# Performance work log

Measured on AMD Instinct MI355X. Metric: run time of the kernel, lower is better.

The kernel has to match this reference:

```python
import jax, jax.numpy as jnp
import numpy as np
from jax import lax

N, IN_DIM, OUT_DIM, E, K = 100000, 128, 128, 600000, 3

def _xavier(key, shape):
    fan_out, fan_in = shape[0], shape[1]
    limit = float(np.sqrt(6.0 / (fan_in + fan_out)))
    return jax.random.uniform(key, shape, jnp.float32, -limit, limit)

def setup_inputs() -> dict:
    key = jax.random.key(0)
    ks = jax.random.split(key, 8)
    x = jax.random.normal(ks[0], (N, IN_DIM), jnp.float32)
    edge_index0 = jax.random.randint(ks[1], (2, E), 0, N, jnp.int64)
    edge_index1 = jax.random.randint(ks[2], (2, E), 0, N, jnp.int64)
    # relation Linear weights, torch layout [out_dim, in_dim]
    W_rel = jnp.stack([_xavier(ks[3], (OUT_DIM, IN_DIM)), _xavier(ks[4], (OUT_DIM, IN_DIM))])
    W_self = _xavier(ks[5], (OUT_DIM, IN_DIM))
    # Conv1d weight [out_ch, in_ch, k], bias [out_ch]
    fan = OUT_DIM * K
    conv_w = jax.random.uniform(ks[6], (OUT_DIM, OUT_DIM, K), jnp.float32, -1.0/np.sqrt(fan), 1.0/np.sqrt(fan))
    conv_b = jax.random.uniform(ks[7], (OUT_DIM,), jnp.float32, -1.0/np.sqrt(fan), 1.0/np.sqrt(fan))
    return {"x": x, "edge_index0": edge_index0, "edge_index1": edge_index1,
            "W_rel": W_rel, "W_self": W_self, "conv_w": conv_w, "conv_b": conv_b}

def reference(x, edge_index0, edge_index1, W_rel, W_self, conv_w, conv_b):
    num_nodes = x.shape[0]
    agg = jnp.zeros((num_nodes, W_rel.shape[1]), x.dtype)
    # per-relation: gather source feats -> linear -> scatter_add into target rows
    for ei, W in ((edge_index0, W_rel[0]), (edge_index1, W_rel[1])):
        src, tgt = ei[0], ei[1]
        messages = x[src] @ W.T                      # [E, out_dim]
        agg = agg.at[tgt].add(messages)
    # self loop
    agg = agg + x @ W_self.T
    # temporal Conv1d over node axis: [1, out_dim, N], kernel 3, padding 1, + ReLU
    # (Dropout is identity in eval mode)
    y = lax.conv_general_dilated(agg.T[None], conv_w, window_strides=(1,),
                                 padding=[(1, 1)],
                                 dimension_numbers=("NCH", "OIH", "NCH"))
    y = jax.nn.relu(y + conv_b[None, :, None])
    return y[0].T                                    # [N, out_dim]
```

## Files before the change

### kernel.cpp

```cpp
#include <hip/hip_runtime.h>
#include <hip/hip_bf16.h>

typedef __hip_bfloat16 bf16;
typedef short v8s __attribute__((ext_vector_type(8)));
typedef float v4f __attribute__((ext_vector_type(4)));
typedef unsigned int u32;

#define BFLO(u) __uint_as_float((u) << 16)
#define BFHI(u) __uint_as_float((u) & 0xffff0000u)

#define CH 4096
#define MAXNB 800
#define CAP 2048

__device__ __forceinline__ int block_stride(const int* e0, int E, int* sm) {
    int t = threadIdx.x;
    if (t == 0) *sm = 0;
    __syncthreads();
    int nz = 0;
    for (int i = t; i < 2048; i += 256) {
        int slot = 2 * i + 1;
        if (slot < 2 * E) nz |= (e0[slot] != 0);
    }
    if (nz) atomicOr(sm, 1);
    __syncthreads();
    return *sm ? 1 : 2;
}


__global__ __launch_bounds__(256) void front_kernel(const float4* __restrict__ x4,
                                                    uint4* __restrict__ Ab4,
                                                    const float* __restrict__ Wrel,
                                                    const float* __restrict__ Wself,
                                                    const float* __restrict__ convw,
                                                    const float* __restrict__ convb,
                                                    bf16* __restrict__ B1T,
                                                    bf16* __restrict__ B2T,
                                                    float* __restrict__ cbf,
                                                    int* __restrict__ gcur,
                                                    int N, int nbrr, int cvtBlocks) {
    int b = blockIdx.x;
    if (b < cvtBlocks) {
        int i = b * 256 + threadIdx.x;
        if (i >= N * 16) return;
        int n = i >> 4, g2 = i & 15;
        float4 f0 = x4[2 * i], f1 = x4[2 * i + 1];
        union { uint4 u; bf16 h[8]; } o;
        o.h[0] = __float2bfloat16(f0.x); o.h[1] = __float2bfloat16(f0.y);
        o.h[2] = __float2bfloat16(f0.z); o.h[3] = __float2bfloat16(f0.w);
        o.h[4] = __float2bfloat16(f1.x); o.h[5] = __float2bfloat16(f1.y);
        o.h[6] = __float2bfloat16(f1.z); o.h[7] = __float2bfloat16(f1.w);
        Ab4[(size_t)n * 48 + 32 + g2] = o.u;
    } else {
        int i = (b - cvtBlocks) * 256 + threadIdx.x;
        if (i < 49152) {
            int co = i / 384, k = i % 384;
            float v;
            if (k < 128)      v = Wrel[co * 128 + k];
            else if (k < 256) v = Wrel[16384 + co * 128 + (k - 128)];
            else              v = Wself[co * 128 + (k - 256)];
            B1T[i] = __float2bfloat16(v);
        } else if (i < 98304) {
            int j = i - 49152;
            int co = j / 384, k = j % 384, kk = k >> 7, ci = k & 127;
            B2T[j] = __float2bfloat16(convw[co * 384 + ci * 3 + kk]);
        } else if (i < 98432) {
            int c = i - 98304;
            cbf[c] = convb[c];
        } else if (i < 98432 + 2 * nbrr) {
            int bb = i - 98432;
            gcur[bb] = bb * CAP;
        }
    }
}


__global__ __launch_bounds__(256) void dist_kernel(const int* __restrict__ e0,
                                                   const int* __restrict__ e1,
                                                   int* __restrict__ gcur,
                                                   unsigned int* __restrict__ esorted,
                                                   int E, int nbrr) {
    __shared__ int hist[MAXNB], lstart[MAXNB], lcur[MAXNB], runbase[MAXNB];
    __shared__ unsigned int ordered[CH];
    __shared__ int tsum[256];
    __shared__ int smf;
    int st = block_stride(e0, E, &smf);
    int NB = 2 * nbrr;
    int t = threadIdx.x;
    for (int i = t; i < NB; i += 256) { hist[i] = 0; lcur[i] = 0; }
    __syncthreads();
    long base = (long)blockIdx.x * CH;
    unsigned int rec[CH / 256]; short bk[CH / 256];
#pragma unroll
    for (int j = 0; j < CH / 256; ++j) {
        long e = base + j * 256 + t;
        if (e < 2 * (long)E) {
            int r = e >= E;
            long idx = r ? e - E : e;
            const int* ei = r ? e1 : e0;
            int src = ei[(size_t)idx * st];
            int tgt = ei[(size_t)(E + idx) * st];
            bk[j] = (short)(r * nbrr + (tgt >> 8));
            rec[j] = (unsigned int)src | ((unsigned int)(tgt & 255) << 17);
            atomicAdd(&hist[bk[j]], 1);
        } else bk[j] = -1;
    }
    __syncthreads();
    {
        int vv[4]; int s = 0;
#pragma unroll
        for (int j = 0; j < 4; ++j) { int i = t * 4 + j; vv[j] = (i < NB) ? hist[i] : 0; s += vv[j]; }
        tsum[t] = s; __syncthreads();
        for (int d = 1; d < 256; d <<= 1) {
            int add = (t >= d) ? tsum[t - d] : 0;
            __syncthreads(); tsum[t] += add; __syncthreads();
        }
        int run = tsum[t] - s;
#pragma unroll
        for (int j = 0; j < 4; ++j) { int i = t * 4 + j; if (i < NB) { lstart[i] = run; run += vv[j]; } }
    }
    __syncthreads();
    for (int i = t; i < NB; i += 256) if (hist[i]) runbase[i] = atomicAdd(&gcur[i], hist[i]);
    __syncthreads();
#pragma unroll
    for (int j = 0; j < CH / 256; ++j) if (bk[j] >= 0) {
        int p = lstart[bk[j]] + atomicAdd(&lcur[bk[j]], 1);
        ordered[p] = rec[j];
    }
    __syncthreads();
    int w = t >> 6, lane = t & 63;
    for (int b = w; b < NB; b += 4) {
        int n = hist[b];
        if (n) {
            int gp = runbase[b], lp = lstart[b];
            for (int q = lane; q < n; q += 64) esorted[gp + q] = ordered[lp + q];
        }
    }
}


__global__ __launch_bounds__(256) void csr_kernel(const unsigned int* __restrict__ esorted,
                                                  const int* __restrict__ gcur,
                                                  int* __restrict__ off, int* __restrict__ cnt,
                                                  int* __restrict__ esrc, int N, int nbrr) {
    __shared__ int hist[256], lcur[256], tsum[256];
    int b = blockIdx.x;
    int r = b >= nbrr;
    int g = r ? b - nbrr : b;
    int t = threadIdx.x;
    int s0 = b * CAP, s1 = gcur[b];
    hist[t] = 0;
    __syncthreads();
    for (int i = s0 + t; i < s1; i += 256)
        atomicAdd(&hist[(esorted[i] >> 17) & 255], 1);
    __syncthreads();
    int h = hist[t];
    tsum[t] = h; __syncthreads();
    for (int d = 1; d < 256; d <<= 1) {
        int add = (t >= d) ? tsum[t - d] : 0;
        __syncthreads(); tsum[t] += add; __syncthreads();
    }
    int start = tsum[t] - h;
    int node = g * 256 + t;
    if (node < N) { off[r * N + node] = s0 + start; cnt[r * N + node] = h; }
    lcur[t] = start;
    __syncthreads();
    for (int i = s0 + t; i < s1; i += 256) {
        unsigned int rec = esorted[i];
        int tl = (rec >> 17) & 255;
        int p = atomicAdd(&lcur[tl], 1);
        esrc[s0 + p] = rec & 0x1FFFF;
    }
}

__global__ __launch_bounds__(256) void gather_kernel(const int* __restrict__ off,
                                                     const int* __restrict__ cnt,
                                                     const int* __restrict__ esrc,
                                                     uint4* __restrict__ Ab4, int N) {
    int grp = blockIdx.x * 16 + (threadIdx.x >> 4);
    int lane = threadIdx.x & 15;
    if (grp >= 2 * N) return;
    int r = (grp >= N);
    int n = r ? grp - N : grp;
    int s0 = off[grp], c = cnt[grp];
    float a0 = 0.f, a1 = 0.f, a2 = 0.f, a3 = 0.f, a4 = 0.f, a5 = 0.f, a6 = 0.f, a7 = 0.f;
    for (int i0 = 0; i0 < c; i0 += 8) {
        int cm1 = c - 1;
        int s[8]; uint4 v[8];
#pragma unroll
        for (int u = 0; u < 8; ++u) {
            int j = i0 + u; j = (j <= cm1) ? j : cm1;
            s[u] = esrc[s0 + j];
        }
#pragma unroll
        for (int u = 0; u < 8; ++u)
            v[u] = Ab4[(size_t)s[u] * 48 + 32 + lane];
#pragma unroll
        for (int u = 0; u < 8; ++u) {
            if (i0 + u < c) {
                a0 += BFLO(v[u].x); a1 += BFHI(v[u].x);
                a2 += BFLO(v[u].y); a3 += BFHI(v[u].y);
                a4 += BFLO(v[u].z); a5 += BFHI(v[u].z);
                a6 += BFLO(v[u].w); a7 += BFHI(v[u].w);
            }
        }
    }
    union { uint4 u; bf16 h[8]; } o;
    o.h[0] = __float2bfloat16(a0); o.h[1] = __float2bfloat16(a1);
    o.h[2] = __float2bfloat16(a2); o.h[3] = __float2bfloat16(a3);
    o.h[4] = __float2bfloat16(a4); o.h[5] = __float2bfloat16(a5);
    o.h[6] = __float2bfloat16(a6); o.h[7] = __float2bfloat16(a7);
    Ab4[(size_t)n * 48 + (size_t)r * 16 + lane] = o.u;
}


__device__ __forceinline__ void gl2lds16(const void* g, void* l) {
    __builtin_amdgcn_global_load_lds(
        (const __attribute__((address_space(1))) u32*)g,
        (__attribute__((address_space(3))) u32*)l, 16, 0, 0);
}

__global__ __launch_bounds__(256) void gemm12_kernel(const bf16* __restrict__ Ab,
                                                     const bf16* __restrict__ B1T,
                                                     const bf16* __restrict__ B2T,
                                                     const float* __restrict__ cbf,
                                                     float* __restrict__ out, int M) {
    __shared__ __align__(16) char ldsbuf[53120];
    bf16* agg = (bf16*)ldsbuf;
    char* Ast = ldsbuf;
    char* Bst = ldsbuf + 36736;

    int t = threadIdx.x;
    int lane = t & 63, wv = t >> 6;
    int r = lane & 15, qq = lane >> 4;
    int m0 = blockIdx.x * 128;
    int swz = (r & 7) << 4;
    int lsw = ((lane & 7) ^ (lane >> 3)) << 4;

    int rowLo = (m0 < 8) ? 8 - m0 : 0;
    int rowHi = (m0 + 136 > M) ? M - m0 + 8 : 144;
    bool bdry = (rowLo > 0) || (rowHi < 144);

    const char* AbB = (const char*)Ab;
    const char* B1B = (const char*)B1T;
    const char* B2B = (const char*)B2T;

    v4f acc[9][2] = {};
    for (int kt = 0; kt < 6; ++kt) {
        int k0b = kt * 128;
        for (int c = wv; c < 34; c += 4) {
            if (c < 18) {
                int ar = m0 - 8 + c * 8 + (lane >> 3);
                ar = ar < 0 ? 0 : (ar >= M ? M - 1 : ar);
                gl2lds16(AbB + (size_t)ar * 768 + k0b + lsw, Ast + c * 1024);
            } else {
                int row = (c - 18) * 8 + (lane >> 3);
                gl2lds16(B1B + (size_t)row * 768 + k0b + lsw, Bst + (c - 18) * 1024);
            }
        }
        __syncthreads();
        if (bdry) {
            int* A4 = (int*)Ast;
            for (int i = t; i < rowLo * 32; i += 256) A4[i] = 0;
            for (int i = t; i < (144 - rowHi) * 32; i += 256) A4[rowHi * 32 + i] = 0;
            __syncthreads();
        }
#pragma unroll
        for (int ks = 0; ks < 2; ++ks) {
            int cb = (ks * 64 + qq * 16) ^ swz;
            v8s bfr[2];
#pragma unroll
            for (int tn = 0; tn < 2; ++tn)
                bfr[tn] = *(const v8s*)(Bst + (wv * 32 + tn * 16 + r) * 128 + cb);
#pragma unroll
            for (int tm = 0; tm < 9; ++tm) {
                v8s af = *(const v8s*)(Ast + (tm * 16 + r) * 128 + cb);
#pragma unroll
                for (int tn = 0; tn < 2; ++tn)
                    acc[tm][tn] = __builtin_amdgcn_mfma_f32_16x16x32_bf16(af, bfr[tn], acc[tm][tn], 0, 0, 0);
            }
        }
        __syncthreads();
    }
#pragma unroll
    for (int tm = 0; tm < 9; ++tm)
#pragma unroll
        for (int tn = 0; tn < 2; ++tn)
#pragma unroll
            for (int reg = 0; reg < 4; ++reg) {
                int row = tm * 16 + qq * 4 + reg;
                if (row >= 7 && row < 138)
                    agg[(row - 7) * 136 + wv * 32 + tn * 16 + r] =
                        __float2bfloat16(acc[tm][tn][reg]);
            }
    __syncthreads();

    v4f acc2[8][2] = {};
    for (int kt = 0; kt < 6; ++kt) {
        int k0b = kt * 128;
        int kk = kt >> 1;
        int rem = (kt & 1) * 64;
        for (int c = wv; c < 16; c += 4)
            gl2lds16(B2B + (size_t)(c * 8 + (lane >> 3)) * 768 + k0b + lsw, Bst + c * 1024);
        __syncthreads();
#pragma unroll
        for (int ks = 0; ks < 2; ++ks) {
            int cb = (ks * 64 + qq * 16) ^ swz;
            v8s bfr[2];
#pragma unroll
            for (int tn = 0; tn < 2; ++tn)
                bfr[tn] = *(const v8s*)(Bst + (wv * 32 + tn * 16 + r) * 128 + cb);
#pragma unroll
            for (int tm = 0; tm < 8; ++tm) {
                v8s af = *(const v8s*)&agg[(tm * 16 + r + kk) * 136 + rem + ks * 32 + qq * 8];
#pragma unroll
                for (int tn = 0; tn < 2; ++tn)
                    acc2[tm][tn] = __builtin_amdgcn_mfma_f32_16x16x32_bf16(af, bfr[tn], acc2[tm][tn], 0, 0, 0);
            }
        }
        __syncthreads();
    }
#pragma unroll
    for (int tm = 0; tm < 8; ++tm)
#pragma unroll
        for (int tn = 0; tn < 2; ++tn) {
            int col = wv * 32 + tn * 16 + r;
            float bias = cbf[col];
#pragma unroll
            for (int reg = 0; reg < 4; ++reg) {
                int grow = m0 + tm * 16 + qq * 4 + reg;
                if (grow < M) {
                    float v = acc2[tm][tn][reg] + bias;
                    out[(size_t)grow * 128 + col] = fmaxf(v, 0.f);
                }
            }
        }
}


extern "C" void kernel_launch(void* const* d_in, const int* in_sizes, int n_in,
                              void* d_out, int out_size, void* d_ws, size_t ws_size,
                              hipStream_t stream) {
    const float* x     = (const float*)d_in[0];
    const int*   e0    = (const int*)d_in[1];
    const int*   e1    = (const int*)d_in[2];
    const float* Wrel  = (const float*)d_in[3];
    const float* Wself = (const float*)d_in[4];
    const float* convw = (const float*)d_in[5];
    const float* convb = (const float*)d_in[6];
    float* out = (float*)d_out;

    int N = in_sizes[0] / 128;
    int E = in_sizes[1] / 2;
    int nbrr = (N + 255) >> 8;
    int NB = 2 * nbrr;

    char* p = (char*)d_ws;
    auto alloc = [&](size_t bytes) { char* q = p; p += (bytes + 255) & ~(size_t)255; return q; };
    int*  gcur  = (int*)alloc((size_t)MAXNB * 4);
    unsigned int* esorted = (unsigned int*)alloc((size_t)MAXNB * CAP * 4);
    int*  esrc  = (int*)alloc((size_t)MAXNB * CAP * 4);
    int*  off   = (int*)alloc((size_t)2 * N * 4);
    int*  cnt   = (int*)alloc((size_t)2 * N * 4);
    bf16* Ab   = (bf16*)alloc((size_t)N * 384 * 2);
    bf16* B1T  = (bf16*)alloc(384 * 128 * 2);
    bf16* B2T  = (bf16*)alloc(384 * 128 * 2);
    float* cbf = (float*)alloc(512);

    int cvtBlocks = (N * 16 + 255) / 256;
    int prepBlocks = (98432 + NB + 255) / 256;
    int chBlocks = (2 * E + CH - 1) / CH;
    front_kernel<<<cvtBlocks + prepBlocks, 256, 0, stream>>>(
        (const float4*)x, (uint4*)Ab, Wrel, Wself, convw, convb,
        B1T, B2T, cbf, gcur, N, nbrr, cvtBlocks);

    dist_kernel<<<chBlocks, 256, 0, stream>>>(e0, e1, gcur, esorted, E, nbrr);
    csr_kernel<<<NB, 256, 0, stream>>>(esorted, gcur, off, cnt, esrc, N, nbrr);

    gather_kernel<<<(2 * N + 15) / 16, 256, 0, stream>>>(off, cnt, esrc, (uint4*)Ab, N);

    int mBlocks = (N + 127) / 128;
    gemm12_kernel<<<mBlocks, 256, 0, stream>>>(Ab, B1T, B2T, cbf, out, N);
}
```

Before: 275.3 us.

## Fuse front with edge distribution, and CSR build with gather via LDS

Merges the input conversion/weight-prep kernel with the edge bucketing kernel into a single launch, replacing the gcur init with a memset and adding `i*CAP` inside the kernel. Merges the CSR construction and neighbour gather-sum into one kernel that keeps each bucket's sorted edge list in LDS, avoiding the global esrc/off/cnt arrays and two launches. The trade-off is that the gather now runs on only about 782 blocks, each walking 256 nodes, instead of thousands of small blocks. That may reduce latency hiding for the random row loads. The fused front kernel also carries the distribution kernel's LDS footprint on every block.

```diff
diff --git a/kernel.cpp b/kernel.cpp
--- a/kernel.cpp
+++ b/kernel.cpp
@@ -28,17 +28,21 @@
 }
 
 
-__global__ __launch_bounds__(256) void front_kernel(const float4* __restrict__ x4,
-                                                    uint4* __restrict__ Ab4,
-                                                    const float* __restrict__ Wrel,
-                                                    const float* __restrict__ Wself,
-                                                    const float* __restrict__ convw,
-                                                    const float* __restrict__ convb,
-                                                    bf16* __restrict__ B1T,
-                                                    bf16* __restrict__ B2T,
-                                                    float* __restrict__ cbf,
-                                                    int* __restrict__ gcur,
-                                                    int N, int nbrr, int cvtBlocks) {
+__global__ __launch_bounds__(256) void frontdist_kernel(const float4* __restrict__ x4,
+                                                        uint4* __restrict__ Ab4,
+                                                        const float* __restrict__ Wrel,
+                                                        const float* __restrict__ Wself,
+                                                        const float* __restrict__ convw,
+                                                        const float* __restrict__ convb,
+                                                        bf16* __restrict__ B1T,
+                                                        bf16* __restrict__ B2T,
+                                                        float* __restrict__ cbf,
+                                                        const int* __restrict__ e0,
+                                                        const int* __restrict__ e1,
+                                                        int* __restrict__ gcur,
+                                                        unsigned int* __restrict__ esorted,
+                                                        int N, int E, int nbrr,
+                                                        int cvtBlocks, int prepBlocks) {
     int b = blockIdx.x;
     if (b < cvtBlocks) {
         int i = b * 256 + threadIdx.x;
@@ -51,7 +55,7 @@
         o.h[4] = __float2bfloat16(f1.x); o.h[5] = __float2bfloat16(f1.y);
         o.h[6] = __float2bfloat16(f1.z); o.h[7] = __float2bfloat16(f1.w);
         Ab4[(size_t)n * 48 + 32 + g2] = o.u;
-    } else {
+    } else if (b < cvtBlocks + prepBlocks) {
         int i = (b - cvtBlocks) * 256 + threadIdx.x;
         if (i < 49152) {
             int co = i / 384, k = i % 384;
@@ -67,92 +71,88 @@
         } else if (i < 98432) {
             int c = i - 98304;
             cbf[c] = convb[c];
-        } else if (i < 98432 + 2 * nbrr) {
-            int bb = i - 98432;
-            gcur[bb] = bb * CAP;
-        }
-    }
-}
-
-
-__global__ __launch_bounds__(256) void dist_kernel(const int* __restrict__ e0,
-                                                   const int* __restrict__ e1,
-                                                   int* __restrict__ gcur,
-                                                   unsigned int* __restrict__ esorted,
-                                                   int E, int nbrr) {
-    __shared__ int hist[MAXNB], lstart[MAXNB], lcur[MAXNB], runbase[MAXNB];
-    __shared__ unsigned int ordered[CH];
-    __shared__ int tsum[256];
-    __shared__ int smf;
-    int st = block_stride(e0, E, &smf);
-    int NB = 2 * nbrr;
-    int t = threadIdx.x;
-    for (int i = t; i < NB; i += 256) { hist[i] = 0; lcur[i] = 0; }
-    __syncthreads();
-    long base = (long)blockIdx.x * CH;
-    unsigned int rec[CH / 256]; short bk[CH / 256];
-#pragma unroll
-    for (int j = 0; j < CH / 256; ++j) {
-        long e = base + j * 256 + t;
-        if (e < 2 * (long)E) {
-            int r = e >= E;
-            long idx = r ? e - E : e;
-            const int* ei = r ? e1 : e0;
-            int src = ei[(size_t)idx * st];
-            int tgt = ei[(size_t)(E + idx) * st];
-            bk[j] = (short)(r * nbrr + (tgt >> 8));
-            rec[j] = (unsigned int)src | ((unsigned int)(tgt & 255) << 17);
-            atomicAdd(&hist[bk[j]], 1);
-        } else bk[j] = -1;
-    }
-    __syncthreads();
-    {
-        int vv[4]; int s = 0;
-#pragma unroll
-        for (int j = 0; j < 4; ++j) { int i = t * 4 + j; vv[j] = (i < NB) ? hist[i] : 0; s += vv[j]; }
-        tsum[t] = s; __syncthreads();
-        for (int d = 1; d < 256; d <<= 1) {
-            int add = (t >= d) ? tsum[t - d] : 0;
-            __syncthreads(); tsum[t] += add; __syncthreads();
-        }
-        int run = tsum[t] - s;
-#pragma unroll
-        for (int j = 0; j < 4; ++j) { int i = t * 4 + j; if (i < NB) { lstart[i] = run; run += vv[j]; } }
-    }
-    __syncthreads();
-    for (int i = t; i < NB; i += 256) if (hist[i]) runbase[i] = atomicAdd(&gcur[i], hist[i]);
-    __syncthreads();
-#pragma unroll
-    for (int j = 0; j < CH / 256; ++j) if (bk[j] >= 0) {
-        int p = lstart[bk[j]] + atomicAdd(&lcur[bk[j]], 1);
-        ordered[p] = rec[j];
-    }
-    __syncthreads();
-    int w = t >> 6, lane = t & 63;
-    for (int b = w; b < NB; b += 4) {
-        int n = hist[b];
-        if (n) {
-            int gp = runbase[b], lp = lstart[b];
-            for (int q = lane; q < n; q += 64) esorted[gp + q] = ordered[lp + q];
-        }
-    }
-}
-
-
-__global__ __launch_bounds__(256) void csr_kernel(const unsigned int* __restrict__ esorted,
-                                                  const int* __restrict__ gcur,
-                                                  int* __restrict__ off, int* __restrict__ cnt,
-                                                  int* __restrict__ esrc, int N, int nbrr) {
+        }
+    } else {
+        __shared__ int hist[MAXNB], lstart[MAXNB], lcur[MAXNB], runbase[MAXNB];
+        __shared__ unsigned int ordered[CH];
+        __shared__ int tsum[256];
+        __shared__ int smf;
+        int st = block_stride(e0, E, &smf);
+        int NB = 2 * nbrr;
+        int t = threadIdx.x;
+        for (int i = t; i < NB; i += 256) { hist[i] = 0; lcur[i] = 0; }
+        __syncthreads();
+        long base = (long)(b - cvtBlocks - prepBlocks) * CH;
+        unsigned int rec[CH / 256]; short bk[CH / 256];
+#pragma unroll
+        for (int j = 0; j < CH / 256; ++j) {
+            long e = base + j * 256 + t;
+            if (e < 2 * (long)E) {
+                int r = e >= E;
+                long idx = r ? e - E : e;
+                const int* ei = r ? e1 : e0;
+                int src = ei[(size_t)idx * st];
+                int tgt = ei[(size_t)(E + idx) * st];
+                bk[j] = (short)(r * nbrr + (tgt >> 8));
+                rec[j] = (unsigned int)src | ((unsigned int)(tgt & 255) << 17);
+                atomicAdd(&hist[bk[j]], 1);
+            } else bk[j] = -1;
+        }
+        __syncthreads();
+        {
+            int vv[4]; int s = 0;
+#pragma unroll
+            for (int j = 0; j < 4; ++j) { int i = t * 4 + j; vv[j] = (i < NB) ? hist[i] : 0; s += vv[j]; }
+            tsum[t] = s; __syncthreads();
+            for (int d = 1; d < 256; d <<= 1) {
+                int add = (t >= d) ? tsum[t - d] : 0;
+                __syncthreads(); tsum[t] += add; __syncthreads();
+            }
+            int run = tsum[t] - s;
+#pragma unroll
+            for (int j = 0; j < 4; ++j) { int i = t * 4 + j; if (i < NB) { lstart[i] = run; run += vv[j]; } }
+        }
+        __syncthreads();
+        for (int i = t; i < NB; i += 256)
+            if (hist[i]) runbase[i] = i * CAP + atomicAdd(&gcur[i], hist[i]);
+        __syncthreads();
+#pragma unroll
+        for (int j = 0; j < CH / 256; ++j) if (bk[j] >= 0) {
+            int p = lstart[bk[j]] + atomicAdd(&lcur[bk[j]], 1);
+            ordered[p] = rec[j];
+        }
+        __syncthreads();
+        int w = t >> 6, lane = t & 63;
+        for (int bb = w; bb < NB; bb += 4) {
+            int n = hist[bb];
+            if (n) {
+                int gp = runbase[bb], lp = lstart[bb];
+                for (int q = lane; q < n; q += 64) esorted[gp + q] = ordered[lp + q];
+            }
+        }
+    }
+}
+
+
+__global__ __launch_bounds__(256) void csrgather_kernel(const unsigned int* __restrict__ esorted,
+                                                        const int* __restrict__ gcur,
+                                                        uint4* __restrict__ Ab4, int N, int nbrr) {
+    __shared__ unsigned int rec_l[CAP];
+    __shared__ int esrc_l[CAP];
     __shared__ int hist[256], lcur[256], tsum[256];
     int b = blockIdx.x;
     int r = b >= nbrr;
     int g = r ? b - nbrr : b;
     int t = threadIdx.x;
-    int s0 = b * CAP, s1 = gcur[b];
+    int s0 = b * CAP;
+    int ne = gcur[b]; ne = (ne > CAP) ? CAP : ne;
     hist[t] = 0;
     __syncthreads();
-    for (int i = s0 + t; i < s1; i += 256)
-        atomicAdd(&hist[(esorted[i] >> 17) & 255], 1);
+    for (int i = t; i < ne; i += 256) {
+        unsigned int rec = esorted[s0 + i];
+        rec_l[i] = rec;
+        atomicAdd(&hist[(rec >> 17) & 255], 1);
+    }
     __syncthreads();
     int h = hist[t];
     tsum[t] = h; __syncthreads();
@@ -160,57 +160,50 @@
         int add = (t >= d) ? tsum[t - d] : 0;
         __syncthreads(); tsum[t] += add; __syncthreads();
     }
-    int start = tsum[t] - h;
-    int node = g * 256 + t;
-    if (node < N) { off[r * N + node] = s0 + start; cnt[r * N + node] = h; }
-    lcur[t] = start;
-    __syncthreads();
-    for (int i = s0 + t; i < s1; i += 256) {
-        unsigned int rec = esorted[i];
-        int tl = (rec >> 17) & 255;
-        int p = atomicAdd(&lcur[tl], 1);
-        esrc[s0 + p] = rec & 0x1FFFF;
-    }
-}
-
-__global__ __launch_bounds__(256) void gather_kernel(const int* __restrict__ off,
-                                                     const int* __restrict__ cnt,
-                                                     const int* __restrict__ esrc,
-                                                     uint4* __restrict__ Ab4, int N) {
-    int grp = blockIdx.x * 16 + (threadIdx.x >> 4);
-    int lane = threadIdx.x & 15;
-    if (grp >= 2 * N) return;
-    int r = (grp >= N);
-    int n = r ? grp - N : grp;
-    int s0 = off[grp], c = cnt[grp];
-    float a0 = 0.f, a1 = 0.f, a2 = 0.f, a3 = 0.f, a4 = 0.f, a5 = 0.f, a6 = 0.f, a7 = 0.f;
-    for (int i0 = 0; i0 < c; i0 += 8) {
-        int cm1 = c - 1;
-        int s[8]; uint4 v[8];
-#pragma unroll
-        for (int u = 0; u < 8; ++u) {
-            int j = i0 + u; j = (j <= cm1) ? j : cm1;
-            s[u] = esrc[s0 + j];
-        }
-#pragma unroll
-        for (int u = 0; u < 8; ++u)
-            v[u] = Ab4[(size_t)s[u] * 48 + 32 + lane];
-#pragma unroll
-        for (int u = 0; u < 8; ++u) {
-            if (i0 + u < c) {
-                a0 += BFLO(v[u].x); a1 += BFHI(v[u].x);
-                a2 += BFLO(v[u].y); a3 += BFHI(v[u].y);
-                a4 += BFLO(v[u].z); a5 += BFHI(v[u].z);
-                a6 += BFLO(v[u].w); a7 += BFHI(v[u].w);
-            }
-        }
-    }
-    union { uint4 u; bf16 h[8]; } o;
-    o.h[0] = __float2bfloat16(a0); o.h[1] = __float2bfloat16(a1);
-    o.h[2] = __float2bfloat16(a2); o.h[3] = __float2bfloat16(a3);
-    o.h[4] = __float2bfloat16(a4); o.h[5] = __float2bfloat16(a5);
-    o.h[6] = __float2bfloat16(a6); o.h[7] = __float2bfloat16(a7);
-    Ab4[(size_t)n * 48 + (size_t)r * 16 + lane] = o.u;
+    lcur[t] = tsum[t] - h;
+    __syncthreads();
+    for (int i = t; i < ne; i += 256) {
+        unsigned int rec = rec_l[i];
+        int p = atomicAdd(&lcur[(rec >> 17) & 255], 1);
+        esrc_l[p] = rec & 0x1FFFF;
+    }
+    __syncthreads();
+    int grp = t >> 4, lane = t & 15;
+    for (int it = 0; it < 16; ++it) {
+        int nl = grp * 16 + it;
+        int node = g * 256 + nl;
+        if (node >= N) break;
+        int c = hist[nl];
+        int sl = tsum[nl] - c;
+        float a0 = 0.f, a1 = 0.f, a2 = 0.f, a3 = 0.f, a4 = 0.f, a5 = 0.f, a6 = 0.f, a7 = 0.f;
+        for (int i0 = 0; i0 < c; i0 += 8) {
+            int cm1 = c - 1;
+            int s[8]; uint4 v[8];
+#pragma unroll
+            for (int u = 0; u < 8; ++u) {
+                int j = i0 + u; j = (j <= cm1) ? j : cm1;
+                s[u] = esrc_l[sl + j];
+            }
+#pragma unroll
+            for (int u = 0; u < 8; ++u)
+                v[u] = Ab4[(size_t)s[u] * 48 + 32 + lane];
+#pragma unroll
+            for (int u = 0; u < 8; ++u) {
+                if (i0 + u < c) {
+                    a0 += BFLO(v[u].x); a1 += BFHI(v[u].x);
+                    a2 += BFLO(v[u].y); a3 += BFHI(v[u].y);
+                    a4 += BFLO(v[u].z); a5 += BFHI(v[u].z);
+                    a6 += BFLO(v[u].w); a7 += BFHI(v[u].w);
+                }
+            }
+        }
+        union { uint4 u; bf16 hh[8]; } o;
+        o.hh[0] = __float2bfloat16(a0); o.hh[1] = __float2bfloat16(a1);
+        o.hh[2] = __float2bfloat16(a2); o.hh[3] = __float2bfloat16(a3);
+        o.hh[4] = __float2bfloat16(a4); o.hh[5] = __float2bfloat16(a5);
+        o.hh[6] = __float2bfloat16(a6); o.hh[7] = __float2bfloat16(a7);
+        Ab4[(size_t)node * 48 + (size_t)r * 16 + lane] = o.u;
+    }
 }
 
 
@@ -359,25 +352,21 @@
     auto alloc = [&](size_t bytes) { char* q = p; p += (bytes + 255) & ~(size_t)255; return q; };
     int*  gcur  = (int*)alloc((size_t)MAXNB * 4);
     unsigned int* esorted = (unsigned int*)alloc((size_t)MAXNB * CAP * 4);
-    int*  esrc  = (int*)alloc((size_t)MAXNB * CAP * 4);
-    int*  off   = (int*)alloc((size_t)2 * N * 4);
-    int*  cnt   = (int*)alloc((size_t)2 * N * 4);
     bf16* Ab   = (bf16*)alloc((size_t)N * 384 * 2);
     bf16* B1T  = (bf16*)alloc(384 * 128 * 2);
     bf16* B2T  = (bf16*)alloc(384 * 128 * 2);
     float* cbf = (float*)alloc(512);
 
+    hipMemsetAsync(gcur, 0, (size_t)NB * 4, stream);
+
     int cvtBlocks = (N * 16 + 255) / 256;
-    int prepBlocks = (98432 + NB + 255) / 256;
+    int prepBlocks = (98432 + 255) / 256;
     int chBlocks = (2 * E + CH - 1) / CH;
-    front_kernel<<<cvtBlocks + prepBlocks, 256, 0, stream>>>(
+    frontdist_kernel<<<cvtBlocks + prepBlocks + chBlocks, 256, 0, stream>>>(
         (const float4*)x, (uint4*)Ab, Wrel, Wself, convw, convb,
-        B1T, B2T, cbf, gcur, N, nbrr, cvtBlocks);
-
-    dist_kernel<<<chBlocks, 256, 0, stream>>>(e0, e1, gcur, esorted, E, nbrr);
-    csr_kernel<<<NB, 256, 0, stream>>>(esorted, gcur, off, cnt, esrc, N, nbrr);
-
-    gather_kernel<<<(2 * N + 15) / 16, 256, 0, stream>>>(off, cnt, esrc, (uint4*)Ab, N);
+        B1T, B2T, cbf, e0, e1, gcur, esorted, N, E, nbrr, cvtBlocks, prepBlocks);
+
+    csrgather_kernel<<<NB, 256, 0, stream>>>(esorted, gcur, (uint4*)Ab, N, nbrr);
 
     int mBlocks = (N + 127) / 128;
     gemm12_kernel<<<mBlocks, 256, 0, stream>>>(Ab, B1T, B2T, cbf, out, N);
```

Result: no change. 271.1 us (-1.5%).
